# Performance work log

Measured on AMD Instinct MI355X. Metric: run time of the kernel, lower is better.

The kernel has to match this reference:

```python
import jax, jax.numpy as jnp
import numpy as np

E = 23   # unique_experts_num
K = 3    # act_experts_num
D = 1024 # in_features
H = 768  # hidden_features (0.75 * dim, per MOEBlock mlp_ratio)


def setup_inputs() -> dict:
    key = jax.random.key(0)
    ks = jax.random.split(key, 12)
    s_in = 1.0 / np.sqrt(D)
    s_hid = 1.0 / np.sqrt(H)
    x = jax.random.normal(ks[0], (4, 1024, D), dtype=jnp.float32)
    gate_W = jax.random.normal(ks[1], (D, E), dtype=jnp.float32) * s_in
    gate_b = jnp.zeros((E,), jnp.float32)
    bias = jnp.zeros((E,), jnp.float32)  # registered buffer, init to zeros
    W1 = jax.random.normal(ks[2], (E, D, H), dtype=jnp.float32) * s_in
    b1 = jnp.zeros((E, H), jnp.float32)
    W2 = jax.random.normal(ks[3], (E, H, D), dtype=jnp.float32) * s_hid
    b2 = jnp.zeros((E, D), jnp.float32)
    sW1 = jax.random.normal(ks[4], (D, H), dtype=jnp.float32) * s_in
    sb1 = jnp.zeros((H,), jnp.float32)
    sW2 = jax.random.normal(ks[5], (H, D), dtype=jnp.float32) * s_hid
    sb2 = jnp.zeros((D,), jnp.float32)
    return {"x": x, "gate_W": gate_W, "gate_b": gate_b, "bias": bias,
            "W1": W1, "b1": b1, "W2": W2, "b2": b2,
            "sW1": sW1, "sb1": sb1, "sW2": sW2, "sb2": sb2}


def reference(x, gate_W, gate_b, bias, W1, b1, W2, b2, sW1, sb1, sW2, sb2):
    o_shape = x.shape
    xt = x.reshape(-1, o_shape[-1])          # [T, D]
    T = xt.shape[0]

    # gating: sigmoid gate, top-k indices chosen on (gate + bias), weights gathered from gate
    gate = jax.nn.sigmoid(xt @ gate_W + gate_b)            # [T, E]
    _, top_idx = jax.lax.top_k(gate + bias, K)             # [T, K]
    top_w = jnp.take_along_axis(gate, top_idx, axis=-1)    # [T, K]
    top_w = top_w / jnp.sum(top_w, axis=-1, keepdims=True)

    # combine matrix: C[t, e] = normalized gate weight if e in top-k of token t else 0
    C = jnp.zeros((T, E), xt.dtype).at[jnp.arange(T)[:, None], top_idx].set(top_w)

    # all-expert dense compute (math-equivalent to dispatch/compute/combine)
    h = jax.nn.gelu(jnp.einsum('td,edh->eth', xt, W1) + b1[:, None, :], approximate=False)
    y = jnp.einsum('eth,ehd->etd', h, W2) + b2[:, None, :]  # [E, T, D]
    moe_out = jnp.einsum('etd,te->td', y, C)                # weighted combine

    # shared expert applied to every token
    shared = jax.nn.gelu(xt @ sW1 + sb1, approximate=False) @ sW2 + sb2
    out = shared + moe_out

    # aux load-balance loss
    gate_norm = gate / jnp.sum(gate, axis=-1, keepdims=True)
    P = jnp.mean(gate_norm, axis=0)                          # [E]
    counts = jnp.sum(jax.nn.one_hot(top_idx, E, dtype=jnp.float32), axis=(0, 1))  # [E]
    F = E * counts / (K * T)
    aux_loss = jnp.sum(P * F)

    return out.reshape(o_shape), aux_loss, counts.astype(jnp.int32)
```

## Files before the change

kernel.cpp:

```cpp
#include <hip/hip_runtime.h>
#include <math.h>

#define TT 4096
#define DD 1024
#define HH 768
#define NE 23
#define NG 24
#define BM 128
#define BN 128
#define BK 64
#define MAXT 160
#define KB1 16
#define KB2 12
#define NY1 6
#define NY2 8
#define NWG1 (MAXT*NY1)
#define NWG2 (MAXT*NY2)
#define CVT1_BLKS 2304
#define CVT_TOT   4608
#define GATE_BLKS 1024

#define WS_CURS   0
#define WS_OFFS   576
#define WS_TOTAL  640
#define WS_T2E    672
#define WS_T2A    832
#define WS_TOKE   1024
#define WS_TOKW   13312
#define WS_LTOK   25600
#define WS_LW     41984
#define WS_PPART  58368
#define WS_CPART  81920
#define WS_SIDX   106496
#define XB_OFF  ((size_t)524288)
#define H_OFF   ((size_t)8912896)
#define W1B_OFF ((size_t)34078720)
#define W2B_OFF ((size_t)71827456)

typedef short bf16x8 __attribute__((ext_vector_type(8)));
typedef float f32x4 __attribute__((ext_vector_type(4)));

#define S_BARRIER() asm volatile("s_barrier" ::: "memory")
#define WAIT_VM0()  asm volatile("s_waitcnt vmcnt(0)" ::: "memory")

__device__ inline unsigned short bfr(float f) {
    unsigned u = __float_as_uint(f);
    u += 0x7fffu + ((u >> 16) & 1u);
    return (unsigned short)(u >> 16);
}
__device__ inline unsigned bfr2(float lo, float hi) {
    return (unsigned)bfr(lo) | ((unsigned)bfr(hi) << 16);
}
__device__ inline float b2f(unsigned short u) {
    return __uint_as_float((unsigned)u << 16);
}

__device__ __forceinline__ void gl_lds16(const void* g, void* l) {
    __builtin_amdgcn_global_load_lds(
        (const __attribute__((address_space(1))) unsigned int*)g,
        (__attribute__((address_space(3))) unsigned int*)l, 16, 0, 0);
}

__global__ __launch_bounds__(256) void k_gatecvt(
    const float* __restrict__ x, const float* __restrict__ gW,
    const float* __restrict__ gb, const float* __restrict__ bias,
    const float* __restrict__ W1, const float* __restrict__ sW1,
    const float* __restrict__ W2, const float* __restrict__ sW2,
    int* __restrict__ tokE, float* __restrict__ tokW,
    float* __restrict__ Ppart, int* __restrict__ Cpart,
    unsigned short* __restrict__ xb,
    unsigned short* __restrict__ W1b, unsigned short* __restrict__ W2b)
{
    __shared__ __align__(16) char smem[16896];
    const int tid = threadIdx.x;

    if (blockIdx.x < CVT_TOT) {
        int id = blockIdx.x;
        const float* src; unsigned short* dst;
        int N, kb0, n0, KBt, e;
        if (id < CVT1_BLKS) {
            N = HH; KBt = KB1;
            n0 = (id % 12) * 64; kb0 = ((id / 12) % 8) * 2; e = id / 96;
            src = (e < NE) ? (W1 + (size_t)e * DD * HH) : sW1;
            dst = W1b;
        } else {
            id -= CVT1_BLKS;
            N = DD; KBt = KB2;
            n0 = (id % 16) * 64; kb0 = ((id / 16) % 6) * 2; e = id / 96;
            src = (e < NE) ? (W2 + (size_t)e * HH * DD) : sW2;
            dst = W2b;
        }
        unsigned (*Ls)[32][65] = (unsigned (*)[32][65])smem;
        const int c = (tid & 15) * 4, r2l = tid >> 4;
        #pragma unroll
        for (int t = 0; t < 2; t++) {
            const float* tsrc = src + (size_t)(kb0 + t) * 64 * N + n0;
            #pragma unroll
            for (int pass = 0; pass < 2; pass++) {
                int row2 = pass * 16 + r2l;
                float4 v0 = *(const float4*)(tsrc + (size_t)(2 * row2) * N + c);
                float4 v1 = *(const float4*)(tsrc + (size_t)(2 * row2 + 1) * N + c);
                uint4 o;
                o.x = bfr2(v0.x, v1.x); o.y = bfr2(v0.y, v1.y);
                o.z = bfr2(v0.z, v1.z); o.w = bfr2(v0.w, v1.w);
                *(uint4*)&Ls[t][row2][c] = o;
            }
        }
        __syncthreads();
        #pragma unroll
        for (int t = 0; t < 2; t++) {
            unsigned short* dbase = dst + ((size_t)(e * KBt + kb0 + t) * N + n0) * 64;
            #pragma unroll
            for (int half = 0; half < 2; half++) {
                int g = half * 256 + tid;
                int n = g >> 3, p = g & 7;
                int j4 = (p ^ (n & 7)) * 4;
                uint4 o;
                o.x = Ls[t][j4 + 0][n]; o.y = Ls[t][j4 + 1][n];
                o.z = Ls[t][j4 + 2][n]; o.w = Ls[t][j4 + 3][n];
                *(uint4*)(dbase + n * 64 + p * 8) = o;
            }
        }
        return;
    }

    float (*xs)[DD] = (float (*)[DD])smem;
    float (*gv)[NE] = (float (*)[NE])(smem + 16384);
    float* ginvs    = (float*)(smem + 16768);
    int (*sel)[3]   = (int (*)[3])(smem + 16784);
    const int bid = blockIdx.x - CVT_TOT;
    const int t0 = bid * 4;
    {
        const float4* srcx = (const float4*)(x + (size_t)t0 * DD);
        float4* dstx = (float4*)&xs[0][0];
        #pragma unroll
        for (int i = 0; i < 4; i++) dstx[tid + 256 * i] = srcx[tid + 256 * i];
    }
    __syncthreads();
    {
        const float* xf = &xs[0][0];
        unsigned short* xd = xb + (size_t)t0 * DD;
        #pragma unroll
        for (int it = 0; it < 4; it++) {
            int o = it * 1024 + tid * 4;
            ushort4 u = make_ushort4(bfr(xf[o]), bfr(xf[o + 1]), bfr(xf[o + 2]), bfr(xf[o + 3]));
            *(ushort4*)(xd + o) = u;
        }
    }
    const int w = tid >> 6, l = tid & 63;
    const int t = t0 + w;
    if (l < NE) {
        float s0 = 0.f, s1 = 0.f, s2 = 0.f, s3 = 0.f;
        const float* xw = xs[w];
        for (int d = 0; d < DD; d += 4) {
            s0 = fmaf(xw[d + 0], gW[(d + 0) * NE + l], s0);
            s1 = fmaf(xw[d + 1], gW[(d + 1) * NE + l], s1);
            s2 = fmaf(xw[d + 2], gW[(d + 2) * NE + l], s2);
            s3 = fmaf(xw[d + 3], gW[(d + 3) * NE + l], s3);
        }
        float s = (s0 + s1) + (s2 + s3) + gb[l];
        gv[w][l] = 1.f / (1.f + expf(-s));
    }
    __syncthreads();
    if (l == 0) {
        unsigned chosen = 0;
        int be[3]; float bw[3];
        float gsum = 0.f;
        for (int e = 0; e < NE; e++) gsum += gv[w][e];
        #pragma unroll
        for (int k = 0; k < 3; k++) {
            float m = -1e30f; int mi = 0;
            for (int e = 0; e < NE; e++) {
                float kv = gv[w][e] + bias[e];
                if (!((chosen >> e) & 1u) && kv > m) { m = kv; mi = e; }
            }
            chosen |= 1u << mi;
            be[k] = mi; bw[k] = gv[w][mi];
        }
        float inv = 1.f / (bw[0] + bw[1] + bw[2]);
        #pragma unroll
        for (int k = 0; k < 3; k++) {
            tokE[t * 3 + k] = be[k];
            tokW[t * 3 + k] = bw[k] * inv;
            sel[w][k] = be[k];
        }
        ginvs[w] = 1.f / gsum;
    }
    __syncthreads();
    if (tid < NE) {
        float p = gv[0][tid] * ginvs[0] + gv[1][tid] * ginvs[1]
                + gv[2][tid] * ginvs[2] + gv[3][tid] * ginvs[3];
        Ppart[tid * 1024 + bid] = p;
        int c = 0;
        #pragma unroll
        for (int w2 = 0; w2 < 4; w2++)
            #pragma unroll
            for (int k = 0; k < 3; k++) c += (sel[w2][k] == tid);
        Cpart[tid * 1024 + bid] = c;
    }
}

__global__ __launch_bounds__(256) void k_reduce(
    const float* __restrict__ Ppart, const int* __restrict__ Cpart,
    int* __restrict__ counts, float* __restrict__ Psum)
{
    const int e = blockIdx.x;
    const int tid = threadIdx.x;
    float s = 0.f; int c = 0;
    for (int i = tid; i < 1024; i += 256) {
        s += Ppart[e * 1024 + i];
        c += Cpart[e * 1024 + i];
    }
    #pragma unroll
    for (int off = 32; off >= 1; off >>= 1) {
        s += __shfl_down(s, off, 64);
        c += __shfl_down(c, off, 64);
    }
    __shared__ float ss[4]; __shared__ int sc[4];
    if ((tid & 63) == 0) { ss[tid >> 6] = s; sc[tid >> 6] = c; }
    __syncthreads();
    if (tid == 0) {
        Psum[e] = ss[0] + ss[1] + ss[2] + ss[3];
        counts[e] = sc[0] + sc[1] + sc[2] + sc[3];
    }
}

__global__ void k_scan(const int* __restrict__ counts, const float* __restrict__ Psum,
                       int* __restrict__ offs, int* __restrict__ total,
                       int* __restrict__ t2e, int* __restrict__ t2a,
                       int* __restrict__ curs, float* __restrict__ outAux)
{
    const int tid = threadIdx.x;
    for (int i = tid; i < NE * 16; i += 256) curs[i] = 0;
    if (tid != 0) return;
    int off = 0, toff = 0;
    for (int e = 0; e < NG; e++) {
        int c = (e < NE) ? counts[e] : TT;
        offs[e] = off;
        int nt = (c + BM - 1) / BM;
        for (int t = 0; t < nt; t++) {
            t2e[toff + t] = e;
            t2a[toff + t] = off + t * BM;
        }
        off += c; toff += nt;
    }
    offs[NG] = off;
    *total = toff;
    float aux = 0.f;
    for (int e = 0; e < NE; e++) {
        float P = Psum[e] / (float)TT;
        float F = (float)NE * (float)counts[e] / (float)(3 * TT);
        aux += P * F;
    }
    outAux[0] = aux;
    for (int e = 0; e < NE; e++) outAux[1 + e] = (float)counts[e];
}

__global__ void k_scatter(const int* __restrict__ tokE, const float* __restrict__ tokW,
                          const int* __restrict__ offs, int* __restrict__ curs,
                          int* __restrict__ ltok, float* __restrict__ lw,
                          int* __restrict__ sidx)
{
    int t = blockIdx.x * 256 + threadIdx.x;
    if (t >= TT) return;
    #pragma unroll
    for (int k = 0; k < 3; k++) {
        int e = tokE[t * 3 + k];
        int pos = atomicAdd(&curs[e * 16], 1);
        int idx = offs[e] + pos;
        ltok[idx] = t; lw[idx] = tokW[t * 3 + k];
        sidx[t * 3 + k] = idx;
    }
    ltok[3 * TT + t] = t;
    lw[3 * TT + t] = 1.f;
}

__global__ __launch_bounds__(256) void k_mm1(
    const unsigned short* __restrict__ xb, const unsigned short* __restrict__ W1b,
    const float* __restrict__ b1, const float* __restrict__ sb1,
    const int* __restrict__ t2e, const int* __restrict__ t2a,
    const int* __restrict__ offs, const int* __restrict__ total,
    const int* __restrict__ ltok, unsigned short* __restrict__ H)
{
    const int id = blockIdx.x;
    const int wg = (id & 7) * (NWG1 / 8) + (id >> 3);
    const int ns = wg / MAXT;
    const int tb = wg % MAXT;
    if (tb >= *total) return;
    const int e = t2e[tb];
    const int a0 = t2a[tb];
    const int acount = min(offs[e + 1] - a0, BM);
    const float* bb = (e < NE) ? (b1 + e * HH) : sb1;
    const int nb = ns * BN;

    __shared__ unsigned short As[2][BM * BK];
    __shared__ unsigned short Bs[2][BN * BK];
    __shared__ int rows[BM];
    const int tid = threadIdx.x;
    if (tid < BM) rows[tid] = ltok[a0 + min(tid, acount - 1)];
    __syncthreads();

    const int wid = tid >> 6, lane = tid & 63;
    const int wr = wid >> 1, wc = wid & 1;
    const int l15 = lane & 15, l4 = lane >> 4;

    float bv[4];
    #pragma unroll
    for (int n = 0; n < 4; n++) bv[n] = bb[nb + wc * 64 + n * 16 + l15];

    f32x4 acc[4][4];
    #pragma unroll
    for (int m = 0; m < 4; m++)
        #pragma unroll
        for (int n = 0; n < 4; n++) acc[m][n] = (f32x4){0.f, 0.f, 0.f, 0.f};

    const unsigned short* aSrc[4];
    int Goff[4];
    #pragma unroll
    for (int c = 0; c < 4; c++) {
        int G = (wid * 4 + c) * 64 + lane;
        int row = G >> 3, j = G & 7;
        aSrc[c] = xb + (size_t)rows[row] * DD + ((j ^ (row & 7)) << 3);
        Goff[c] = G * 8;
    }
    const unsigned short* wbase = W1b + ((size_t)e * KB1 * HH + nb) * 64;

    auto stage = [&](int buf, int kb) {
        #pragma unroll
        for (int c = 0; c < 4; c++)
            gl_lds16(aSrc[c] + kb * 64, &As[buf][Goff[c]]);
        const unsigned short* wb = wbase + (size_t)kb * (HH * 64);
        #pragma unroll
        for (int c = 0; c < 4; c++)
            gl_lds16(wb + Goff[c], &Bs[buf][Goff[c]]);
    };
    auto compute = [&](int buf) {
        #pragma unroll
        for (int kh = 0; kh < 2; kh++) {
            bf16x8 af[4], bf[4];
            #pragma unroll
            for (int f = 0; f < 4; f++) {
                int ar = wr * 64 + f * 16 + l15;
                int br = wc * 64 + f * 16 + l15;
                int pg = (kh << 2) + l4;
                af[f] = *(const bf16x8*)&As[buf][ar * 64 + ((pg ^ (ar & 7)) << 3)];
                bf[f] = *(const bf16x8*)&Bs[buf][br * 64 + ((pg ^ (br & 7)) << 3)];
            }
            #pragma unroll
            for (int m = 0; m < 4; m++)
                #pragma unroll
                for (int n = 0; n < 4; n++)
                    acc[m][n] = __builtin_amdgcn_mfma_f32_16x16x32_bf16(af[m], bf[n], acc[m][n], 0, 0, 0);
        }
    };

    stage(0, 0);
    WAIT_VM0();
    S_BARRIER();
    int cur = 0;
    #pragma unroll 1
    for (int kb = 0; kb < KB1; kb++) {
        if (kb + 1 < KB1) stage(cur ^ 1, kb + 1);
        __builtin_amdgcn_sched_barrier(0);
        compute(cur);
        if (kb + 1 < KB1) {
            WAIT_VM0();
            S_BARRIER();
            cur ^= 1;
        }
    }

    #pragma unroll
    for (int m = 0; m < 4; m++) {
        int rbase = wr * 64 + m * 16 + l4 * 4;
        #pragma unroll
        for (int n = 0; n < 4; n++) {
            int col = nb + wc * 64 + n * 16 + l15;
            #pragma unroll
            for (int i = 0; i < 4; i++) {
                int r = rbase + i;
                if (r < acount) {
                    float v = acc[m][n][i] + bv[n];
                    float u = v + 0.044715f * v * v * v;
                    float g = v / (1.f + __expf(-1.5957691216f * u));
                    H[(size_t)(a0 + r) * HH + col] = bfr(g);
                }
            }
        }
    }
}

__global__ __launch_bounds__(256) void k_mm2(
    const unsigned short* __restrict__ H, const unsigned short* __restrict__ W2b,
    const float* __restrict__ b2, const float* __restrict__ sb2,
    const int* __restrict__ t2e, const int* __restrict__ t2a,
    const int* __restrict__ offs, const int* __restrict__ total,
    const int* __restrict__ ltok, const float* __restrict__ lw,
    unsigned short* __restrict__ yslot, float* __restrict__ out)
{
    const int id = blockIdx.x;
    const int wg = (id & 7) * (NWG2 / 8) + (id >> 3);
    const int ns = wg / MAXT;
    const int tb = wg % MAXT;
    if (tb >= *total) return;
    const int e = t2e[tb];
    const int a0 = t2a[tb];
    const int acount = min(offs[e + 1] - a0, BM);
    const float* bb = (e < NE) ? (b2 + e * DD) : sb2;
    const int nb = ns * BN;

    __shared__ unsigned short As[2][BM * BK];
    __shared__ unsigned short Bs[2][BN * BK];
    __shared__ int rows[BM];
    __shared__ float wts[BM];
    const int tid = threadIdx.x;
    if (tid < BM) {
        rows[tid] = (tid < acount) ? ltok[a0 + tid] : -1;
        wts[tid]  = (tid < acount) ? lw[a0 + tid] : 0.f;
    }
    __syncthreads();

    const int wid = tid >> 6, lane = tid & 63;
    const int wr = wid >> 1, wc = wid & 1;
    const int l15 = lane & 15, l4 = lane >> 4;

    float bv[4];
    #pragma unroll
    for (int n = 0; n < 4; n++) bv[n] = bb[nb + wc * 64 + n * 16 + l15];

    f32x4 acc[4][4];
    #pragma unroll
    for (int m = 0; m < 4; m++)
        #pragma unroll
        for (int n = 0; n < 4; n++) acc[m][n] = (f32x4){0.f, 0.f, 0.f, 0.f};

    const unsigned short* aSrc[4];
    int Goff[4];
    #pragma unroll
    for (int c = 0; c < 4; c++) {
        int G = (wid * 4 + c) * 64 + lane;
        int row = G >> 3, j = G & 7;
        aSrc[c] = H + (size_t)(a0 + row) * HH + ((j ^ (row & 7)) << 3);
        Goff[c] = G * 8;
    }
    const unsigned short* wbase = W2b + ((size_t)e * KB2 * DD + nb) * 64;

    auto stage = [&](int buf, int kb) {
        #pragma unroll
        for (int c = 0; c < 4; c++)
            gl_lds16(aSrc[c] + kb * 64, &As[buf][Goff[c]]);
        const unsigned short* wb = wbase + (size_t)kb * (DD * 64);
        #pragma unroll
        for (int c = 0; c < 4; c++)
            gl_lds16(wb + Goff[c], &Bs[buf][Goff[c]]);
    };
    auto compute = [&](int buf) {
        #pragma unroll
        for (int kh = 0; kh < 2; kh++) {
            bf16x8 af[4], bf[4];
            #pragma unroll
            for (int f = 0; f < 4; f++) {
                int ar = wr * 64 + f * 16 + l15;
                int br = wc * 64 + f * 16 + l15;
                int pg = (kh << 2) + l4;
                af[f] = *(const bf16x8*)&As[buf][ar * 64 + ((pg ^ (ar & 7)) << 3)];
                bf[f] = *(const bf16x8*)&Bs[buf][br * 64 + ((pg ^ (br & 7)) << 3)];
            }
            #pragma unroll
            for (int m = 0; m < 4; m++)
                #pragma unroll
                for (int n = 0; n < 4; n++)
                    acc[m][n] = __builtin_amdgcn_mfma_f32_16x16x32_bf16(af[m], bf[n], acc[m][n], 0, 0, 0);
        }
    };

    stage(0, 0);
    WAIT_VM0();
    S_BARRIER();
    int cur = 0;
    #pragma unroll 1
    for (int kb = 0; kb < KB2; kb++) {
        if (kb + 1 < KB2) stage(cur ^ 1, kb + 1);
        __builtin_amdgcn_sched_barrier(0);
        compute(cur);
        if (kb + 1 < KB2) {
            WAIT_VM0();
            S_BARRIER();
            cur ^= 1;
        }
    }

    if (e == NE) {
        #pragma unroll
        for (int m = 0; m < 4; m++) {
            int rbase = wr * 64 + m * 16 + l4 * 4;
            #pragma unroll
            for (int n = 0; n < 4; n++) {
                int col = nb + wc * 64 + n * 16 + l15;
                #pragma unroll
                for (int i = 0; i < 4; i++) {
                    int r = rbase + i;
                    out[(size_t)rows[r] * DD + col] = acc[m][n][i] + bv[n];
                }
            }
        }
    } else {
        #pragma unroll
        for (int m = 0; m < 4; m++) {
            int rbase = wr * 64 + m * 16 + l4 * 4;
            #pragma unroll
            for (int n = 0; n < 4; n++) {
                int col = nb + wc * 64 + n * 16 + l15;
                #pragma unroll
                for (int i = 0; i < 4; i++) {
                    int r = rbase + i;
                    if (r < acount)
                        yslot[(size_t)(a0 + r) * DD + col] = bfr(wts[r] * (acc[m][n][i] + bv[n]));
                }
            }
        }
    }
}

__global__ __launch_bounds__(256) void k_combine(
    const unsigned short* __restrict__ yslot, const int* __restrict__ sidx,
    float* __restrict__ out)
{
    const int t = blockIdx.x;
    const int s0 = sidx[t * 3 + 0], s1 = sidx[t * 3 + 1], s2 = sidx[t * 3 + 2];
    const int d = threadIdx.x * 4;
    float* o = out + (size_t)t * DD + d;
    float4 v = *(float4*)o;
    ushort4 a = *(const ushort4*)(yslot + (size_t)s0 * DD + d);
    ushort4 b = *(const ushort4*)(yslot + (size_t)s1 * DD + d);
    ushort4 c = *(const ushort4*)(yslot + (size_t)s2 * DD + d);
    v.x += b2f(a.x) + b2f(b.x) + b2f(c.x);
    v.y += b2f(a.y) + b2f(b.y) + b2f(c.y);
    v.z += b2f(a.z) + b2f(b.z) + b2f(c.z);
    v.w += b2f(a.w) + b2f(b.w) + b2f(c.w);
    *(float4*)o = v;
}

extern "C" void kernel_launch(void* const* d_in, const int* in_sizes, int n_in,
                              void* d_out, int out_size, void* d_ws, size_t ws_size,
                              hipStream_t stream)
{
    const float* x    = (const float*)d_in[0];
    const float* gW   = (const float*)d_in[1];
    const float* gb   = (const float*)d_in[2];
    const float* bias = (const float*)d_in[3];
    const float* W1   = (const float*)d_in[4];
    const float* b1   = (const float*)d_in[5];
    const float* W2   = (const float*)d_in[6];
    const float* b2   = (const float*)d_in[7];
    const float* sW1  = (const float*)d_in[8];
    const float* sb1  = (const float*)d_in[9];
    const float* sW2  = (const float*)d_in[10];
    const float* sb2  = (const float*)d_in[11];
    float* out = (float*)d_out;
    float* wsf = (float*)d_ws;
    int*   wsi = (int*)d_ws;

    int*   curs   = wsi + WS_CURS;
    int*   offs   = wsi + WS_OFFS;
    int*   total  = wsi + WS_TOTAL;
    int*   t2e    = wsi + WS_T2E;
    int*   t2a    = wsi + WS_T2A;
    int*   tokE   = wsi + WS_TOKE;
    float* tokW   = wsf + WS_TOKW;
    int*   ltok   = wsi + WS_LTOK;
    float* lwt    = wsf + WS_LW;
    float* Ppart  = wsf + WS_PPART;
    int*   Cpart  = wsi + WS_CPART;
    int*   sidx   = wsi + WS_SIDX;
    int*   counts = wsi + 432;
    float* Psum   = wsf + 464;
    unsigned short* xb  = (unsigned short*)((char*)d_ws + XB_OFF);
    unsigned short* Hb  = (unsigned short*)((char*)d_ws + H_OFF);
    unsigned short* W1b = (unsigned short*)((char*)d_ws + W1B_OFF);
    unsigned short* W2b = (unsigned short*)((char*)d_ws + W2B_OFF);
    unsigned short* yslot = W1b;

    k_gatecvt<<<CVT_TOT + GATE_BLKS, 256, 0, stream>>>(
        x, gW, gb, bias, W1, sW1, W2, sW2, tokE, tokW, Ppart, Cpart, xb, W1b, W2b);
    k_reduce<<<NE, 256, 0, stream>>>(Ppart, Cpart, counts, Psum);
    k_scan<<<1, 256, 0, stream>>>(counts, Psum, offs, total, t2e, t2a, curs,
                                  out + (size_t)TT * DD);
    k_scatter<<<TT / 256, 256, 0, stream>>>(tokE, tokW, offs, curs, ltok, lwt, sidx);
    k_mm1<<<NWG1, 256, 0, stream>>>(xb, W1b, b1, sb1, t2e, t2a, offs, total, ltok, Hb);
    k_mm2<<<NWG2, 256, 0, stream>>>(Hb, W2b, b2, sb2, t2e, t2a, offs, total, ltok, lwt,
                                    yslot, out);
    k_combine<<<TT, 256, 0, stream>>>(yslot, sidx, out);
}
```

Baseline: 225.5 us.

## Split gate from weight conversion and parallelize gate GEMV across wave lanes

The gating work moves out of the fused convert kernel into its own kernel. In it, each lane of a wave holds a 16-element slice of the token's activations and multiplies it against all 24 (padded) expert columns, then the partial sums are reduced with wave shuffles. The old version used only 23 lanes per wave, each running a serial 1024-long dot product. A few extra blocks in the convert kernel write a padded, float4-aligned copy of the gate weights into scratch space that aliases the H buffer. The cost is one more kernel launch and a 24-accumulator shuffle reduction per wave.

```diff
diff --git a/kernel.cpp b/kernel.cpp
--- a/kernel.cpp
+++ b/kernel.cpp
@@ -18,7 +18,7 @@
 #define NWG2 (MAXT*NY2)
 #define CVT1_BLKS 2304
 #define CVT_TOT   4608
-#define GATE_BLKS 1024
+#define PAD_BLKS  24
 
 #define WS_CURS   0
 #define WS_OFFS   576
@@ -61,121 +61,143 @@
         (__attribute__((address_space(3))) unsigned int*)l, 16, 0, 0);
 }
 
-__global__ __launch_bounds__(256) void k_gatecvt(
-    const float* __restrict__ x, const float* __restrict__ gW,
-    const float* __restrict__ gb, const float* __restrict__ bias,
+__global__ __launch_bounds__(256) void k_cvt(
     const float* __restrict__ W1, const float* __restrict__ sW1,
     const float* __restrict__ W2, const float* __restrict__ sW2,
+    const float* __restrict__ gW,
+    unsigned short* __restrict__ W1b, unsigned short* __restrict__ W2b,
+    float* __restrict__ gWp)
+{
+    const int tid = threadIdx.x;
+    if (blockIdx.x >= CVT_TOT) {
+        int i0 = (blockIdx.x - CVT_TOT) * 1024 + tid * 4;
+        float4 o;
+        float v[4];
+        #pragma unroll
+        for (int q = 0; q < 4; q++) {
+            int idx = i0 + q;
+            int d = idx / 24, e = idx % 24;
+            v[q] = (e < NE) ? gW[d * NE + e] : 0.f;
+        }
+        o.x = v[0]; o.y = v[1]; o.z = v[2]; o.w = v[3];
+        *(float4*)(gWp + i0) = o;
+        return;
+    }
+    int id = blockIdx.x;
+    const float* src; unsigned short* dst;
+    int N, kb0, n0, KBt, e;
+    if (id < CVT1_BLKS) {
+        N = HH; KBt = KB1;
+        n0 = (id % 12) * 64; kb0 = ((id / 12) % 8) * 2; e = id / 96;
+        src = (e < NE) ? (W1 + (size_t)e * DD * HH) : sW1;
+        dst = W1b;
+    } else {
+        id -= CVT1_BLKS;
+        N = DD; KBt = KB2;
+        n0 = (id % 16) * 64; kb0 = ((id / 16) % 6) * 2; e = id / 96;
+        src = (e < NE) ? (W2 + (size_t)e * HH * DD) : sW2;
+        dst = W2b;
+    }
+    __shared__ unsigned Ls[2][32][65];
+    const int c = (tid & 15) * 4, r2l = tid >> 4;
+    #pragma unroll
+    for (int t = 0; t < 2; t++) {
+        const float* tsrc = src + (size_t)(kb0 + t) * 64 * N + n0;
+        #pragma unroll
+        for (int pass = 0; pass < 2; pass++) {
+            int row2 = pass * 16 + r2l;
+            float4 v0 = *(const float4*)(tsrc + (size_t)(2 * row2) * N + c);
+            float4 v1 = *(const float4*)(tsrc + (size_t)(2 * row2 + 1) * N + c);
+            uint4 o;
+            o.x = bfr2(v0.x, v1.x); o.y = bfr2(v0.y, v1.y);
+            o.z = bfr2(v0.z, v1.z); o.w = bfr2(v0.w, v1.w);
+            *(uint4*)&Ls[t][row2][c] = o;
+        }
+    }
+    __syncthreads();
+    #pragma unroll
+    for (int t = 0; t < 2; t++) {
+        unsigned short* dbase = dst + ((size_t)(e * KBt + kb0 + t) * N + n0) * 64;
+        #pragma unroll
+        for (int half = 0; half < 2; half++) {
+            int g = half * 256 + tid;
+            int n = g >> 3, p = g & 7;
+            int j4 = (p ^ (n & 7)) * 4;
+            uint4 o;
+            o.x = Ls[t][j4 + 0][n]; o.y = Ls[t][j4 + 1][n];
+            o.z = Ls[t][j4 + 2][n]; o.w = Ls[t][j4 + 3][n];
+            *(uint4*)(dbase + n * 64 + p * 8) = o;
+        }
+    }
+}
+
+__global__ __launch_bounds__(256) void k_gate2(
+    const float* __restrict__ x, const float* __restrict__ gWp,
+    const float* __restrict__ gb, const float* __restrict__ bias,
     int* __restrict__ tokE, float* __restrict__ tokW,
     float* __restrict__ Ppart, int* __restrict__ Cpart,
-    unsigned short* __restrict__ xb,
-    unsigned short* __restrict__ W1b, unsigned short* __restrict__ W2b)
-{
-    __shared__ __align__(16) char smem[16896];
+    unsigned short* __restrict__ xb)
+{
+    __shared__ float gv[4][24];
+    __shared__ float ginvs[4];
+    __shared__ int sel[4][3];
     const int tid = threadIdx.x;
-
-    if (blockIdx.x < CVT_TOT) {
-        int id = blockIdx.x;
-        const float* src; unsigned short* dst;
-        int N, kb0, n0, KBt, e;
-        if (id < CVT1_BLKS) {
-            N = HH; KBt = KB1;
-            n0 = (id % 12) * 64; kb0 = ((id / 12) % 8) * 2; e = id / 96;
-            src = (e < NE) ? (W1 + (size_t)e * DD * HH) : sW1;
-            dst = W1b;
-        } else {
-            id -= CVT1_BLKS;
-            N = DD; KBt = KB2;
-            n0 = (id % 16) * 64; kb0 = ((id / 16) % 6) * 2; e = id / 96;
-            src = (e < NE) ? (W2 + (size_t)e * HH * DD) : sW2;
-            dst = W2b;
-        }
-        unsigned (*Ls)[32][65] = (unsigned (*)[32][65])smem;
-        const int c = (tid & 15) * 4, r2l = tid >> 4;
-        #pragma unroll
-        for (int t = 0; t < 2; t++) {
-            const float* tsrc = src + (size_t)(kb0 + t) * 64 * N + n0;
-            #pragma unroll
-            for (int pass = 0; pass < 2; pass++) {
-                int row2 = pass * 16 + r2l;
-                float4 v0 = *(const float4*)(tsrc + (size_t)(2 * row2) * N + c);
-                float4 v1 = *(const float4*)(tsrc + (size_t)(2 * row2 + 1) * N + c);
-                uint4 o;
-                o.x = bfr2(v0.x, v1.x); o.y = bfr2(v0.y, v1.y);
-                o.z = bfr2(v0.z, v1.z); o.w = bfr2(v0.w, v1.w);
-                *(uint4*)&Ls[t][row2][c] = o;
-            }
-        }
-        __syncthreads();
-        #pragma unroll
-        for (int t = 0; t < 2; t++) {
-            unsigned short* dbase = dst + ((size_t)(e * KBt + kb0 + t) * N + n0) * 64;
-            #pragma unroll
-            for (int half = 0; half < 2; half++) {
-                int g = half * 256 + tid;
-                int n = g >> 3, p = g & 7;
-                int j4 = (p ^ (n & 7)) * 4;
-                uint4 o;
-                o.x = Ls[t][j4 + 0][n]; o.y = Ls[t][j4 + 1][n];
-                o.z = Ls[t][j4 + 2][n]; o.w = Ls[t][j4 + 3][n];
-                *(uint4*)(dbase + n * 64 + p * 8) = o;
-            }
-        }
-        return;
-    }
-
-    float (*xs)[DD] = (float (*)[DD])smem;
-    float (*gv)[NE] = (float (*)[NE])(smem + 16384);
-    float* ginvs    = (float*)(smem + 16768);
-    int (*sel)[3]   = (int (*)[3])(smem + 16784);
-    const int bid = blockIdx.x - CVT_TOT;
-    const int t0 = bid * 4;
+    const int w = tid >> 6, l = tid & 63;
+    const int t = blockIdx.x * 4 + w;
+
+    float xr[16];
     {
-        const float4* srcx = (const float4*)(x + (size_t)t0 * DD);
-        float4* dstx = (float4*)&xs[0][0];
-        #pragma unroll
-        for (int i = 0; i < 4; i++) dstx[tid + 256 * i] = srcx[tid + 256 * i];
-    }
-    __syncthreads();
-    {
-        const float* xf = &xs[0][0];
-        unsigned short* xd = xb + (size_t)t0 * DD;
-        #pragma unroll
-        for (int it = 0; it < 4; it++) {
-            int o = it * 1024 + tid * 4;
-            ushort4 u = make_ushort4(bfr(xf[o]), bfr(xf[o + 1]), bfr(xf[o + 2]), bfr(xf[o + 3]));
-            *(ushort4*)(xd + o) = u;
-        }
-    }
-    const int w = tid >> 6, l = tid & 63;
-    const int t = t0 + w;
-    if (l < NE) {
-        float s0 = 0.f, s1 = 0.f, s2 = 0.f, s3 = 0.f;
-        const float* xw = xs[w];
-        for (int d = 0; d < DD; d += 4) {
-            s0 = fmaf(xw[d + 0], gW[(d + 0) * NE + l], s0);
-            s1 = fmaf(xw[d + 1], gW[(d + 1) * NE + l], s1);
-            s2 = fmaf(xw[d + 2], gW[(d + 2) * NE + l], s2);
-            s3 = fmaf(xw[d + 3], gW[(d + 3) * NE + l], s3);
-        }
-        float s = (s0 + s1) + (s2 + s3) + gb[l];
-        gv[w][l] = 1.f / (1.f + expf(-s));
-    }
-    __syncthreads();
+        const float* xs = x + (size_t)t * DD + l * 16;
+        #pragma unroll
+        for (int i = 0; i < 4; i++) {
+            float4 v = *(const float4*)(xs + 4 * i);
+            xr[4*i] = v.x; xr[4*i+1] = v.y; xr[4*i+2] = v.z; xr[4*i+3] = v.w;
+        }
+        unsigned xo[8];
+        #pragma unroll
+        for (int i = 0; i < 8; i++) xo[i] = bfr2(xr[2*i], xr[2*i+1]);
+        unsigned short* xd = xb + (size_t)t * DD + l * 16;
+        *(uint4*)xd       = make_uint4(xo[0], xo[1], xo[2], xo[3]);
+        *(uint4*)(xd + 8) = make_uint4(xo[4], xo[5], xo[6], xo[7]);
+    }
+
+    float acc[24];
+    #pragma unroll
+    for (int e = 0; e < 24; e++) acc[e] = 0.f;
+    const float* gr = gWp + (size_t)l * 16 * 24;
+    #pragma unroll
+    for (int j = 0; j < 16; j++) {
+        float g[24];
+        #pragma unroll
+        for (int q = 0; q < 6; q++) {
+            float4 v = *(const float4*)(gr + j * 24 + q * 4);
+            g[4*q] = v.x; g[4*q+1] = v.y; g[4*q+2] = v.z; g[4*q+3] = v.w;
+        }
+        #pragma unroll
+        for (int e = 0; e < 24; e++) acc[e] = fmaf(xr[j], g[e], acc[e]);
+    }
+    #pragma unroll
+    for (int e = 0; e < 24; e++) {
+        #pragma unroll
+        for (int off = 32; off >= 1; off >>= 1)
+            acc[e] += __shfl_down(acc[e], off, 64);
+    }
     if (l == 0) {
-        unsigned chosen = 0;
-        int be[3]; float bw[3];
-        float gsum = 0.f;
-        for (int e = 0; e < NE; e++) gsum += gv[w][e];
+        float sg[23]; float gsum = 0.f;
+        #pragma unroll
+        for (int e = 0; e < NE; e++) {
+            float s = 1.f / (1.f + expf(-(acc[e] + gb[e])));
+            sg[e] = s; gv[w][e] = s; gsum += s;
+        }
+        unsigned chosen = 0; int be[3]; float bw[3];
         #pragma unroll
         for (int k = 0; k < 3; k++) {
             float m = -1e30f; int mi = 0;
             for (int e = 0; e < NE; e++) {
-                float kv = gv[w][e] + bias[e];
+                float kv = sg[e] + bias[e];
                 if (!((chosen >> e) & 1u) && kv > m) { m = kv; mi = e; }
             }
-            chosen |= 1u << mi;
-            be[k] = mi; bw[k] = gv[w][mi];
+            chosen |= 1u << mi; be[k] = mi; bw[k] = sg[mi];
         }
         float inv = 1.f / (bw[0] + bw[1] + bw[2]);
         #pragma unroll
@@ -190,13 +212,13 @@
     if (tid < NE) {
         float p = gv[0][tid] * ginvs[0] + gv[1][tid] * ginvs[1]
                 + gv[2][tid] * ginvs[2] + gv[3][tid] * ginvs[3];
-        Ppart[tid * 1024 + bid] = p;
+        Ppart[tid * 1024 + blockIdx.x] = p;
         int c = 0;
         #pragma unroll
         for (int w2 = 0; w2 < 4; w2++)
             #pragma unroll
             for (int k = 0; k < 3; k++) c += (sel[w2][k] == tid);
-        Cpart[tid * 1024 + bid] = c;
+        Cpart[tid * 1024 + blockIdx.x] = c;
     }
 }
 
@@ -577,12 +599,13 @@
     float* Psum   = wsf + 464;
     unsigned short* xb  = (unsigned short*)((char*)d_ws + XB_OFF);
     unsigned short* Hb  = (unsigned short*)((char*)d_ws + H_OFF);
+    float* gWp = (float*)((char*)d_ws + H_OFF);
     unsigned short* W1b = (unsigned short*)((char*)d_ws + W1B_OFF);
     unsigned short* W2b = (unsigned short*)((char*)d_ws + W2B_OFF);
     unsigned short* yslot = W1b;
 
-    k_gatecvt<<<CVT_TOT + GATE_BLKS, 256, 0, stream>>>(
-        x, gW, gb, bias, W1, sW1, W2, sW2, tokE, tokW, Ppart, Cpart, xb, W1b, W2b);
+    k_cvt<<<CVT_TOT + PAD_BLKS, 256, 0, stream>>>(W1, sW1, W2, sW2, gW, W1b, W2b, gWp);
+    k_gate2<<<TT / 4, 256, 0, stream>>>(x, gWp, gb, bias, tokE, tokW, Ppart, Cpart, xb);
     k_reduce<<<NE, 256, 0, stream>>>(Ppart, Cpart, counts, Psum);
     k_scan<<<1, 256, 0, stream>>>(counts, Psum, offs, total, t2e, t2a, curs,
                                   out + (size_t)TT * DD);
```

After: 240.8 us. +6.8%, slower.
